# Kernel tuning notes

Hardware: AMD Instinct MI355X
Metric: run time of the kernel (lower is better)

Reference implementation:

```python
import jax, jax.numpy as jnp
import numpy as np

N_HEAD, D_K = 8, 16

def _ln(x, g, b):
    m = jnp.mean(x, -1, keepdims=True)
    v = jnp.var(x, -1, keepdims=True)
    return (x - m) * jax.lax.rsqrt(v + 1e-5) * g + b

def _enc_layer(x, wq, bq, wk, bk, wv, bv, wo, bo, g1, be1, cw1, cb1, cw2, cb2, g2, be2):
    B, L, D = x.shape
    q = (x @ wq + bq).reshape(B, L, N_HEAD, D_K)
    k = (x @ wk + bk).reshape(B, L, N_HEAD, D_K)
    v = (x @ wv + bv).reshape(B, L, N_HEAD, D_K)
    attn = jnp.einsum('blhd,bmhd->bhlm', q, k) / jnp.sqrt(jnp.float32(D_K))
    attn = jax.nn.softmax(attn, axis=-1)
    o = jnp.einsum('bhlm,bmhd->blhd', attn, v).reshape(B, L, -1)
    x = _ln(o @ wo + bo + x, g1, be1)          # post-LN residual (MHA)
    h = jax.nn.relu(x @ cw1 + cb1)             # 1x1 conv == linear
    return _ln(h @ cw2 + cb2 + x, g2, be2)     # post-LN residual (FFN)

def setup_inputs() -> dict:
    key = jax.random.key(0)
    ks = jax.random.split(key, 20)
    N, D, NNZ = 100000, 128, 2000000
    B, L, NL, DI = 32, 256, 2, 512
    s = 0.02
    inp = {}
    inp['ego'] = jax.random.normal(ks[0], (N, D), jnp.float32)
    inp['vals'] = jax.random.uniform(ks[1], (NNZ,), jnp.float32) / 20.0  # ~normalized adj values
    inp['W1'] = jax.random.normal(ks[2], (D, D), jnp.float32) * s
    inp['b1'] = jnp.zeros((D,), jnp.float32)
    inp['W2'] = jax.random.normal(ks[3], (D, D), jnp.float32) * s
    inp['b2'] = jnp.zeros((D,), jnp.float32)
    inp['enc_in'] = jax.random.normal(ks[4], (B, L, D), jnp.float32)
    inp['wq'] = jax.random.normal(ks[5], (NL, D, D), jnp.float32) * s
    inp['bq'] = jnp.zeros((NL, D), jnp.float32)
    inp['wk'] = jax.random.normal(ks[6], (NL, D, D), jnp.float32) * s
    inp['bk'] = jnp.zeros((NL, D), jnp.float32)
    inp['wv'] = jax.random.normal(ks[7], (NL, D, D), jnp.float32) * s
    inp['bv'] = jnp.zeros((NL, D), jnp.float32)
    inp['wo'] = jax.random.normal(ks[8], (NL, D, D), jnp.float32) * s
    inp['bo'] = jnp.zeros((NL, D), jnp.float32)
    inp['ln1_g'] = jnp.ones((NL, D), jnp.float32)
    inp['ln1_b'] = jnp.zeros((NL, D), jnp.float32)
    inp['cw1'] = jax.random.normal(ks[9], (NL, D, DI), jnp.float32) * s
    inp['cb1'] = jnp.zeros((NL, DI), jnp.float32)
    inp['cw2'] = jax.random.normal(ks[10], (NL, DI, D), jnp.float32) * s
    inp['cb2'] = jnp.zeros((NL, D), jnp.float32)
    inp['ln2_g'] = jnp.ones((NL, D), jnp.float32)
    inp['ln2_b'] = jnp.zeros((NL, D), jnp.float32)
    inp['rows'] = jnp.sort(jax.random.randint(ks[11], (NNZ,), 0, N, jnp.int32))
    inp['cols'] = jax.random.randint(ks[12], (NNZ,), 0, N, jnp.int32)
    return inp

def reference(ego, vals, W1, b1, W2, b2, enc_in, wq, bq, wk, bk, wv, bv, wo, bo,
              ln1_g, ln1_b, cw1, cb1, cw2, cb2, ln2_g, ln2_b, rows, cols):
    N = ego.shape[0]
    # sparse A_in @ ego  (COO SpMM via gather + segment_sum)
    side = jax.ops.segment_sum(vals[:, None] * ego[cols], rows, num_segments=N)
    # bi-interaction aggregator (dropout=identity in eval)
    sum_emb = jax.nn.leaky_relu((ego + side) @ W1 + b1)
    bi_emb = jax.nn.leaky_relu((ego * side) @ W2 + b2)
    agg = sum_emb + bi_emb
    # transformer encoder over edge sequences
    x = enc_in
    for i in range(wq.shape[0]):
        x = _enc_layer(x, wq[i], bq[i], wk[i], bk[i], wv[i], bv[i], wo[i], bo[i],
                       ln1_g[i], ln1_b[i], cw1[i], cb1[i], cw2[i], cb2[i], ln2_g[i], ln2_b[i])
    return (agg, x)
```

## Files before the change

kernel.cpp:

```cpp
#include <hip/hip_runtime.h>

typedef __attribute__((ext_vector_type(8))) short bf16x8;
typedef __attribute__((ext_vector_type(4))) float f32x4;

__device__ __forceinline__ unsigned short f2b(float f) {
    union { float f; unsigned int i; } u; u.f = f;
    return (unsigned short)((u.i + 0x7FFFu + ((u.i >> 16) & 1u)) >> 16);
}
__device__ __forceinline__ unsigned int packbf2(float a, float b) {
    return (unsigned int)f2b(a) | ((unsigned int)f2b(b) << 16);
}

__device__ __forceinline__ void spmm_block(
    const unsigned int* __restrict__ egob, const float* __restrict__ vals,
    const int* __restrict__ rows, const int* __restrict__ cols,
    float* __restrict__ side, int nnz, int blk)
{
    int tid = threadIdx.x;
    int wave = tid >> 6, lane = tid & 63;
    int e0 = blk * 256 + wave * 64;
    if (e0 >= nnz) return;

    int idx = e0 + lane;
    int last = nnz - 1;
    bool ok = idx < nnz;
    int safe = ok ? idx : last;
    int my_row = rows[safe];
    int my_col = cols[safe];
    float my_val = ok ? vals[safe] : 0.f;

    unsigned int pre[16];
    #pragma unroll
    for (int j = 0; j < 16; ++j) {
        unsigned int c = (unsigned int)__builtin_amdgcn_readlane(my_col, j);
        pre[j] = *(egob + ((size_t)c << 6) + lane);
    }

    float ax = 0.f, ay = 0.f;
    int cur = __builtin_amdgcn_readlane(my_row, 0);
    #pragma unroll
    for (int e = 0; e < 64; ++e) {
        int r = __builtin_amdgcn_readlane(my_row, e);
        float vv = __int_as_float(__builtin_amdgcn_readlane(__float_as_int(my_val), e));
        unsigned int u = pre[e & 15];
        if (e < 48) {
            unsigned int c = (unsigned int)__builtin_amdgcn_readlane(my_col, e + 16);
            pre[e & 15] = *(egob + ((size_t)c << 6) + lane);
        }
        if (r != cur) {
            atomicAdd(&side[(size_t)cur * 128 + lane * 2], ax);
            atomicAdd(&side[(size_t)cur * 128 + lane * 2 + 1], ay);
            ax = 0.f; ay = 0.f; cur = r;
        }
        ax = fmaf(vv, __uint_as_float(u << 16), ax);
        ay = fmaf(vv, __uint_as_float(u & 0xFFFF0000u), ay);
    }
    atomicAdd(&side[(size_t)cur * 128 + lane * 2], ax);
    atomicAdd(&side[(size_t)cur * 128 + lane * 2 + 1], ay);
}

#define LDAB 40

__device__ __forceinline__ void gemm2_core(
    const float* __restrict__ A, const float* __restrict__ W,
    const float* __restrict__ bias, const float* __restrict__ R,
    const float* __restrict__ g, const float* __restrict__ bta,
    float* __restrict__ C, int M, int N, int K, int act,
    int bm, int bn, unsigned short* As, unsigned short* Bs,
    float* redS, float* redSS)
{
    int tid = threadIdx.x, wave = tid >> 6, lane = tid & 63;
    int lm = lane & 15, quad = lane >> 4;
    int wm = wave >> 1, wn = wave & 1;

    f32x4 acc[2][4];
    #pragma unroll
    for (int i = 0; i < 2; ++i)
        #pragma unroll
        for (int j = 0; j < 4; ++j) acc[i][j] = (f32x4)(0.f);

    for (int k0 = 0; k0 < K; k0 += 32) {
        {
            int m = tid >> 2, kc = (tid & 3) * 8;
            const float* p = A + (size_t)(bm + m) * K + k0 + kc;
            float4 a0 = *(const float4*)p, a1 = *(const float4*)(p + 4);
            uint4 pk;
            pk.x = packbf2(a0.x, a0.y); pk.y = packbf2(a0.z, a0.w);
            pk.z = packbf2(a1.x, a1.y); pk.w = packbf2(a1.z, a1.w);
            *(uint4*)&As[m * LDAB + kc] = pk;
        }
        {
            int nn = tid & 127, kh = (tid >> 7) * 16;
            const float* p = W + (size_t)(k0 + kh) * N + bn + nn;
            float w[16];
            #pragma unroll
            for (int j = 0; j < 16; ++j) w[j] = p[(size_t)j * N];
            uint4 pk;
            pk.x = packbf2(w[0], w[1]);  pk.y = packbf2(w[2], w[3]);
            pk.z = packbf2(w[4], w[5]);  pk.w = packbf2(w[6], w[7]);
            *(uint4*)&Bs[nn * LDAB + kh] = pk;
            pk.x = packbf2(w[8], w[9]);  pk.y = packbf2(w[10], w[11]);
            pk.z = packbf2(w[12], w[13]); pk.w = packbf2(w[14], w[15]);
            *(uint4*)&Bs[nn * LDAB + kh + 8] = pk;
        }
        __syncthreads();
        bf16x8 af[2], bfr[4];
        #pragma unroll
        for (int mi = 0; mi < 2; ++mi)
            af[mi] = *(bf16x8*)&As[(wm * 32 + mi * 16 + lm) * LDAB + quad * 8];
        #pragma unroll
        for (int ni = 0; ni < 4; ++ni)
            bfr[ni] = *(bf16x8*)&Bs[(wn * 64 + ni * 16 + lm) * LDAB + quad * 8];
        #pragma unroll
        for (int mi = 0; mi < 2; ++mi)
            #pragma unroll
            for (int ni = 0; ni < 4; ++ni)
                acc[mi][ni] = __builtin_amdgcn_mfma_f32_16x16x32_bf16(
                    af[mi], bfr[ni], acc[mi][ni], 0, 0, 0);
        __syncthreads();
    }

    #pragma unroll
    for (int mi = 0; mi < 2; ++mi) {
        #pragma unroll
        for (int r = 0; r < 4; ++r) {
            int row = bm + wm * 32 + mi * 16 + quad * 4 + r;
            #pragma unroll
            for (int ni = 0; ni < 4; ++ni) {
                int col = bn + wn * 64 + ni * 16 + lm;
                float v = acc[mi][ni][r] + bias[col];
                if (R) v += R[(size_t)row * N + col];
                if (act) v = fmaxf(v, 0.f);
                acc[mi][ni][r] = v;
            }
        }
    }

    if (g) {
        #pragma unroll
        for (int mi = 0; mi < 2; ++mi) {
            #pragma unroll
            for (int r = 0; r < 4; ++r) {
                float s = 0.f, ss = 0.f;
                #pragma unroll
                for (int ni = 0; ni < 4; ++ni) {
                    float v = acc[mi][ni][r];
                    s += v; ss = fmaf(v, v, ss);
                }
                #pragma unroll
                for (int off = 1; off < 16; off <<= 1) {
                    s  += __shfl_xor(s, off, 64);
                    ss += __shfl_xor(ss, off, 64);
                }
                if (lm == 0) {
                    int lr = wm * 32 + mi * 16 + quad * 4 + r;
                    redS[wn * 64 + lr] = s;
                    redSS[wn * 64 + lr] = ss;
                }
            }
        }
        __syncthreads();
        #pragma unroll
        for (int mi = 0; mi < 2; ++mi) {
            #pragma unroll
            for (int r = 0; r < 4; ++r) {
                int lr = wm * 32 + mi * 16 + quad * 4 + r;
                int row = bm + lr;
                float s = redS[lr] + redS[64 + lr];
                float ss = redSS[lr] + redSS[64 + lr];
                float mean = s * (1.f / 128.f);
                float var = ss * (1.f / 128.f) - mean * mean;
                float rstd = rsqrtf(var + 1e-5f);
                #pragma unroll
                for (int ni = 0; ni < 4; ++ni) {
                    int col = wn * 64 + ni * 16 + lm;
                    float y = (acc[mi][ni][r] - mean) * rstd * g[col] + bta[col];
                    C[(size_t)row * 128 + col] = y;
                }
            }
        }
    } else {
        #pragma unroll
        for (int mi = 0; mi < 2; ++mi) {
            #pragma unroll
            for (int r = 0; r < 4; ++r) {
                int row = bm + wm * 32 + mi * 16 + quad * 4 + r;
                #pragma unroll
                for (int ni = 0; ni < 4; ++ni) {
                    int col = bn + wn * 64 + ni * 16 + lm;
                    C[(size_t)row * N + col] = acc[mi][ni][r];
                }
            }
        }
    }
}

__device__ __forceinline__ void bi_core2(
    const float* __restrict__ ego, const float* __restrict__ side,
    const float* __restrict__ W1, const float* __restrict__ b1,
    const float* __restrict__ W2, const float* __restrict__ b2,
    float* __restrict__ out, int M, int bm,
    unsigned short* Us, unsigned short* Ms,
    unsigned short* W1s, unsigned short* W2s)
{
    int tid = threadIdx.x, wave = tid >> 6, lane = tid & 63;
    int lm = lane & 15, quad = lane >> 4;
    int wm = wave >> 1, wn = wave & 1;

    f32x4 acc1[2][4], acc2[2][4];
    #pragma unroll
    for (int i = 0; i < 2; ++i)
        #pragma unroll
        for (int j = 0; j < 4; ++j) { acc1[i][j] = (f32x4)(0.f); acc2[i][j] = (f32x4)(0.f); }

    for (int k0 = 0; k0 < 128; k0 += 32) {
        {
            int m = tid >> 2, kc = (tid & 3) * 8;
            int gm = bm + m;
            float e[8], s[8];
            if (gm < M) {
                const float* pe = ego + (size_t)gm * 128 + k0 + kc;
                const float* ps = side + (size_t)gm * 128 + k0 + kc;
                float4 e0 = *(const float4*)pe, e1 = *(const float4*)(pe + 4);
                float4 s0 = *(const float4*)ps, s1 = *(const float4*)(ps + 4);
                e[0]=e0.x; e[1]=e0.y; e[2]=e0.z; e[3]=e0.w;
                e[4]=e1.x; e[5]=e1.y; e[6]=e1.z; e[7]=e1.w;
                s[0]=s0.x; s[1]=s0.y; s[2]=s0.z; s[3]=s0.w;
                s[4]=s1.x; s[5]=s1.y; s[6]=s1.z; s[7]=s1.w;
            } else {
                #pragma unroll
                for (int j = 0; j < 8; ++j) { e[j] = 0.f; s[j] = 0.f; }
            }
            uint4 pu, pm;
            pu.x = packbf2(e[0]+s[0], e[1]+s[1]); pu.y = packbf2(e[2]+s[2], e[3]+s[3]);
            pu.z = packbf2(e[4]+s[4], e[5]+s[5]); pu.w = packbf2(e[6]+s[6], e[7]+s[7]);
            pm.x = packbf2(e[0]*s[0], e[1]*s[1]); pm.y = packbf2(e[2]*s[2], e[3]*s[3]);
            pm.z = packbf2(e[4]*s[4], e[5]*s[5]); pm.w = packbf2(e[6]*s[6], e[7]*s[7]);
            *(uint4*)&Us[m * LDAB + kc] = pu;
            *(uint4*)&Ms[m * LDAB + kc] = pm;
        }
        {
            int nn = tid & 127, kh = (tid >> 7) * 16;
            const float* p1 = W1 + (size_t)(k0 + kh) * 128 + nn;
            const float* p2 = W2 + (size_t)(k0 + kh) * 128 + nn;
            float wa[16], wb[16];
            #pragma unroll
            for (int j = 0; j < 16; ++j) { wa[j] = p1[(size_t)j * 128]; wb[j] = p2[(size_t)j * 128]; }
            uint4 pk;
            pk.x = packbf2(wa[0], wa[1]);  pk.y = packbf2(wa[2], wa[3]);
            pk.z = packbf2(wa[4], wa[5]);  pk.w = packbf2(wa[6], wa[7]);
            *(uint4*)&W1s[nn * LDAB + kh] = pk;
            pk.x = packbf2(wa[8], wa[9]);  pk.y = packbf2(wa[10], wa[11]);
            pk.z = packbf2(wa[12], wa[13]); pk.w = packbf2(wa[14], wa[15]);
            *(uint4*)&W1s[nn * LDAB + kh + 8] = pk;
            pk.x = packbf2(wb[0], wb[1]);  pk.y = packbf2(wb[2], wb[3]);
            pk.z = packbf2(wb[4], wb[5]);  pk.w = packbf2(wb[6], wb[7]);
            *(uint4*)&W2s[nn * LDAB + kh] = pk;
            pk.x = packbf2(wb[8], wb[9]);  pk.y = packbf2(wb[10], wb[11]);
            pk.z = packbf2(wb[12], wb[13]); pk.w = packbf2(wb[14], wb[15]);
            *(uint4*)&W2s[nn * LDAB + kh + 8] = pk;
        }
        __syncthreads();
        bf16x8 au[2], am[2], bf1[4], bf2[4];
        #pragma unroll
        for (int mi = 0; mi < 2; ++mi) {
            au[mi] = *(bf16x8*)&Us[(wm * 32 + mi * 16 + lm) * LDAB + quad * 8];
            am[mi] = *(bf16x8*)&Ms[(wm * 32 + mi * 16 + lm) * LDAB + quad * 8];
        }
        #pragma unroll
        for (int ni = 0; ni < 4; ++ni) {
            bf1[ni] = *(bf16x8*)&W1s[(wn * 64 + ni * 16 + lm) * LDAB + quad * 8];
            bf2[ni] = *(bf16x8*)&W2s[(wn * 64 + ni * 16 + lm) * LDAB + quad * 8];
        }
        #pragma unroll
        for (int mi = 0; mi < 2; ++mi)
            #pragma unroll
            for (int ni = 0; ni < 4; ++ni) {
                acc1[mi][ni] = __builtin_amdgcn_mfma_f32_16x16x32_bf16(
                    au[mi], bf1[ni], acc1[mi][ni], 0, 0, 0);
                acc2[mi][ni] = __builtin_amdgcn_mfma_f32_16x16x32_bf16(
                    am[mi], bf2[ni], acc2[mi][ni], 0, 0, 0);
            }
        __syncthreads();
    }
    #pragma unroll
    for (int mi = 0; mi < 2; ++mi) {
        #pragma unroll
        for (int r = 0; r < 4; ++r) {
            int row = bm + wm * 32 + mi * 16 + quad * 4 + r;
            if (row < M) {
                #pragma unroll
                for (int ni = 0; ni < 4; ++ni) {
                    int col = wn * 64 + ni * 16 + lm;
                    float v1 = acc1[mi][ni][r] + b1[col];
                    v1 = v1 > 0.f ? v1 : 0.01f * v1;
                    float v2 = acc2[mi][ni][r] + b2[col];
                    v2 = v2 > 0.f ? v2 : 0.01f * v2;
                    out[(size_t)row * 128 + col] = v1 + v2;
                }
            }
        }
    }
}


__global__ __launch_bounds__(256) void qkv2_pre(
    const float* __restrict__ A,
    const float* __restrict__ wq, const float* __restrict__ wk, const float* __restrict__ wv,
    const float* __restrict__ bq, const float* __restrict__ bk, const float* __restrict__ bv,
    float* __restrict__ Q, float* __restrict__ Ko, float* __restrict__ V, int M, int encGy,
    float* __restrict__ side, int Nn,
    const float* __restrict__ ego, unsigned int* __restrict__ egob,
    int encN, int ZB, int CB)
{
    __shared__ unsigned short As[64 * LDAB];
    __shared__ unsigned short Bs[128 * LDAB];
    __shared__ float redS[128], redSS[128];
    int gid = blockIdx.x;
    int tid = threadIdx.x;
    if (gid >= encN) {
        int j = gid - encN;
        if (j < ZB) {
            size_t n4 = (size_t)Nn * 32;
            float4 z = make_float4(0.f, 0.f, 0.f, 0.f);
            for (size_t i = (size_t)j * 256 + tid; i < n4; i += (size_t)ZB * 256)
                ((float4*)side)[i] = z;
        } else {
            int c = j - ZB;
            size_t n4 = (size_t)Nn * 32;
            for (size_t i = (size_t)c * 256 + tid; i < n4; i += (size_t)CB * 256) {
                float4 a = *(const float4*)(ego + i * 4);
                uint2 p;
                p.x = packbf2(a.x, a.y);
                p.y = packbf2(a.z, a.w);
                *(uint2*)(egob + i * 2) = p;
            }
        }
        return;
    }
    int sel = gid / encGy, by = gid % encGy;
    const float* W = (sel == 0) ? wq : (sel == 1) ? wk : wv;
    const float* b = (sel == 0) ? bq : (sel == 1) ? bk : bv;
    float* C = (sel == 0) ? Q : (sel == 1) ? Ko : V;
    gemm2_core(A, W, b, nullptr, nullptr, nullptr, C, M, 128, 128, 0,
               by * 64, 0, As, Bs, redS, redSS);
}

__global__ __launch_bounds__(256) void qkv2_spmm(
    const float* __restrict__ A,
    const float* __restrict__ wq, const float* __restrict__ wk, const float* __restrict__ wv,
    const float* __restrict__ bq, const float* __restrict__ bk, const float* __restrict__ bv,
    float* __restrict__ Q, float* __restrict__ Ko, float* __restrict__ V, int M, int encGy,
    const unsigned int* __restrict__ egob, const float* __restrict__ vals,
    const int* __restrict__ rows, const int* __restrict__ cols,
    float* __restrict__ side, int nnz, int spmmBase, int encN)
{
    __shared__ unsigned short As[64 * LDAB];
    __shared__ unsigned short Bs[128 * LDAB];
    __shared__ float redS[128], redSS[128];
    int gid = blockIdx.x;
    if (gid >= encN) {
        spmm_block(egob, vals, rows, cols, side, nnz, spmmBase + gid - encN);
        return;
    }
    int sel = gid / encGy, by = gid % encGy;
    const float* W = (sel == 0) ? wq : (sel == 1) ? wk : wv;
    const float* b = (sel == 0) ? bq : (sel == 1) ? bk : bv;
    float* C = (sel == 0) ? Q : (sel == 1) ? Ko : V;
    gemm2_core(A, W, b, nullptr, nullptr, nullptr, C, M, 128, 128, 0,
               by * 64, 0, As, Bs, redS, redSS);
}

__global__ __launch_bounds__(256) void gemm2_spmm(
    const float* __restrict__ A, const float* __restrict__ W,
    const float* __restrict__ bias, const float* __restrict__ R,
    const float* __restrict__ g, const float* __restrict__ bta,
    float* __restrict__ C, int M, int N, int K, int act, int encGy,
    const unsigned int* __restrict__ egob, const float* __restrict__ vals,
    const int* __restrict__ rows, const int* __restrict__ cols,
    float* __restrict__ side, int nnz, int spmmBase, int encN)
{
    __shared__ unsigned short As[64 * LDAB];
    __shared__ unsigned short Bs[128 * LDAB];
    __shared__ float redS[128], redSS[128];
    int gid = blockIdx.x;
    if (gid >= encN) {
        spmm_block(egob, vals, rows, cols, side, nnz, spmmBase + gid - encN);
        return;
    }
    int bx = gid / encGy, by = gid % encGy;
    gemm2_core(A, W, bias, R, g, bta, C, M, N, K, act,
               by * 64, bx * 128, As, Bs, redS, redSS);
}

__global__ __launch_bounds__(256) void gemm2_bi2(
    const float* __restrict__ A, const float* __restrict__ W,
    const float* __restrict__ bias, const float* __restrict__ R,
    const float* __restrict__ g, const float* __restrict__ bta,
    float* __restrict__ C, int M, int N, int K, int act, int encGy, int encN,
    const float* __restrict__ ego, const float* __restrict__ side,
    const float* __restrict__ W1, const float* __restrict__ b1,
    const float* __restrict__ W2, const float* __restrict__ b2,
    float* __restrict__ out, int Mbi, int biBase)
{
    __shared__ char smem[30720];
    int gid = blockIdx.x;
    if (gid < encN) {
        unsigned short* As = (unsigned short*)smem;
        unsigned short* Bs = (unsigned short*)(smem + 5120);
        float* redS  = (float*)(smem + 15360);
        float* redSS = (float*)(smem + 15360 + 512);
        int bx = gid / encGy, by = gid % encGy;
        gemm2_core(A, W, bias, R, g, bta, C, M, N, K, act,
                   by * 64, bx * 128, As, Bs, redS, redSS);
    } else {
        int bb = biBase + (gid - encN);
        unsigned short* Us  = (unsigned short*)smem;
        unsigned short* Ms  = (unsigned short*)(smem + 5120);
        unsigned short* W1s = (unsigned short*)(smem + 10240);
        unsigned short* W2s = (unsigned short*)(smem + 20480);
        bi_core2(ego, side, W1, b1, W2, b2, out, Mbi, bb * 64, Us, Ms, W1s, W2s);
    }
}

__device__ __forceinline__ void attn_block(
    const float* __restrict__ q, const float* __restrict__ k,
    const float* __restrict__ v, float* __restrict__ o, int NH,
    int bh, float* Ks, float* Vs)
{
    const int L = 256, DK = 16;
    int b = bh / NH, h = bh % NH;
    int tid = threadIdx.x;

    size_t qbase = ((size_t)(b * L + tid) * NH + h) * DK;
    float qr[16];
    #pragma unroll
    for (int d4 = 0; d4 < 4; ++d4) {
        float4 t = *(const float4*)(q + qbase + d4 * 4);
        qr[d4*4+0] = t.x * 0.25f; qr[d4*4+1] = t.y * 0.25f;
        qr[d4*4+2] = t.z * 0.25f; qr[d4*4+3] = t.w * 0.25f;
    }
    float acc[16];
    #pragma unroll
    for (int d = 0; d < 16; ++d) acc[d] = 0.f;
    float mmax = -1e30f, ssum = 0.f;

    for (int c0 = 0; c0 < L; c0 += 128) {
        __syncthreads();
        for (int i = tid; i < 128 * 4; i += 256) {
            int ll = i >> 2, d4 = (i & 3) * 4;
            size_t gg = ((size_t)(b * L + c0 + ll) * NH + h) * DK + d4;
            *(float4*)&Ks[ll * 16 + d4] = *(const float4*)(k + gg);
            *(float4*)&Vs[ll * 16 + d4] = *(const float4*)(v + gg);
        }
        __syncthreads();

        for (int kk = 0; kk < 128; ++kk) {
            float dot = 0.f;
            #pragma unroll
            for (int d4 = 0; d4 < 4; ++d4) {
                float4 kv = *(const float4*)&Ks[kk * 16 + d4 * 4];
                dot = fmaf(qr[d4*4+0], kv.x, dot);
                dot = fmaf(qr[d4*4+1], kv.y, dot);
                dot = fmaf(qr[d4*4+2], kv.z, dot);
                dot = fmaf(qr[d4*4+3], kv.w, dot);
            }
            if (dot > mmax) {
                float alpha = __expf(mmax - dot);
                ssum *= alpha;
                #pragma unroll
                for (int d = 0; d < 16; ++d) acc[d] *= alpha;
                mmax = dot;
            }
            float p = __expf(dot - mmax);
            ssum += p;
            #pragma unroll
            for (int d4 = 0; d4 < 4; ++d4) {
                float4 vv = *(const float4*)&Vs[kk * 16 + d4 * 4];
                acc[d4*4+0] = fmaf(p, vv.x, acc[d4*4+0]);
                acc[d4*4+1] = fmaf(p, vv.y, acc[d4*4+1]);
                acc[d4*4+2] = fmaf(p, vv.z, acc[d4*4+2]);
                acc[d4*4+3] = fmaf(p, vv.w, acc[d4*4+3]);
            }
        }
    }
    float inv = 1.f / ssum;
    #pragma unroll
    for (int d4 = 0; d4 < 4; ++d4) {
        float4 t;
        t.x = acc[d4*4+0] * inv; t.y = acc[d4*4+1] * inv;
        t.z = acc[d4*4+2] * inv; t.w = acc[d4*4+3] * inv;
        *(float4*)(o + qbase + d4 * 4) = t;
    }
}

__global__ __launch_bounds__(256) void attn_spmm(
    const float* __restrict__ q, const float* __restrict__ k,
    const float* __restrict__ v, float* __restrict__ o, int NH,
    const unsigned int* __restrict__ egob, const float* __restrict__ vals,
    const int* __restrict__ rows, const int* __restrict__ cols,
    float* __restrict__ side, int nnz, int spmmBase, int encN)
{
    __shared__ float Ks[128 * 16];
    __shared__ float Vs[128 * 16];
    int gid = blockIdx.x;
    if (gid >= encN) {
        spmm_block(egob, vals, rows, cols, side, nnz, spmmBase + gid - encN);
        return;
    }
    attn_block(q, k, v, o, NH, gid, Ks, Vs);
}

extern "C" void kernel_launch(void* const* d_in, const int* in_sizes, int n_in,
                              void* d_out, int out_size, void* d_ws, size_t ws_size,
                              hipStream_t stream) {
    const float* ego    = (const float*)d_in[0];
    const float* vals   = (const float*)d_in[1];
    const float* W1     = (const float*)d_in[2];
    const float* b1     = (const float*)d_in[3];
    const float* W2     = (const float*)d_in[4];
    const float* b2     = (const float*)d_in[5];
    const float* enc_in = (const float*)d_in[6];
    const float* wq  = (const float*)d_in[7];
    const float* bq  = (const float*)d_in[8];
    const float* wk  = (const float*)d_in[9];
    const float* bk  = (const float*)d_in[10];
    const float* wv  = (const float*)d_in[11];
    const float* bv  = (const float*)d_in[12];
    const float* wo  = (const float*)d_in[13];
    const float* bo  = (const float*)d_in[14];
    const float* ln1_g = (const float*)d_in[15];
    const float* ln1_b = (const float*)d_in[16];
    const float* cw1 = (const float*)d_in[17];
    const float* cb1 = (const float*)d_in[18];
    const float* cw2 = (const float*)d_in[19];
    const float* cb2 = (const float*)d_in[20];
    const float* ln2_g = (const float*)d_in[21];
    const float* ln2_b = (const float*)d_in[22];
    const int* rows = (const int*)d_in[23];
    const int* cols = (const int*)d_in[24];

    const int D = 128, DI = 512, NH = 8, L = 256;
    const int Nn   = in_sizes[0] / D;
    const int nnz  = in_sizes[1];
    const int NL   = in_sizes[7] / (D * D);
    const int Menc = in_sizes[6] / D;
    const int Bb   = Menc / L;

    float* ws = (float*)d_ws;
    size_t off = 0;
    float* side = ws + off; off += (size_t)Nn * D;
    float* Qb = ws + off; off += (size_t)Menc * D;
    float* Kb = ws + off; off += (size_t)Menc * D;
    float* Vb = ws + off; off += (size_t)Menc * D;
    float* Ob = ws + off; off += (size_t)Menc * D;
    float* XA = ws + off; off += (size_t)Menc * D;
    float* XB = ws + off; off += (size_t)Menc * D;
    float* Hb = ws + off; off += (size_t)Menc * DI;
    unsigned int* egob = (unsigned int*)(ws + off); off += (size_t)Nn * (D / 2);

    float* outAgg = (float*)d_out;
    float* outX   = (float*)d_out + (size_t)Nn * D;

    const int spmmBlocks = (nnz + 255) / 256;
    const int nSpmmStages = 5 * NL - 3;
    const int perS = (spmmBlocks + nSpmmStages - 1) / nSpmmStages;
    const int biTiles = (Nn + 63) / 64;
    const int perB = (biTiles + 1) / 2;
    const int biStart = 5 * NL - 1;
    const int encGy = Menc / 64;
    const int ZB = 512, CB = 1024;
    int sidx = 0, sci = 0, bci = 0;

    const float* x = enc_in;
    for (int i = 0; i < NL; ++i) {
        const size_t wOff = (size_t)i * D * D;
        int base, cnt;
        #define SPMM_CHUNK base = sci * perS; cnt = spmmBlocks - base; \
                           if (cnt < 0) cnt = 0; if (cnt > perS) cnt = perS; sci++
        #define BI_CHUNK   base = bci * perB; cnt = biTiles - base; \
                           if (cnt < 0) cnt = 0; if (cnt > perB) cnt = perB; bci++

        sidx++;
        if (sidx == 1) {
            qkv2_pre<<<3 * encGy + ZB + CB, 256, 0, stream>>>(
                x, wq + wOff, wk + wOff, wv + wOff,
                bq + (size_t)i * D, bk + (size_t)i * D, bv + (size_t)i * D,
                Qb, Kb, Vb, Menc, encGy,
                side, Nn, ego, egob, 3 * encGy, ZB, CB);
        } else {
            SPMM_CHUNK;
            qkv2_spmm<<<3 * encGy + cnt, 256, 0, stream>>>(
                x, wq + wOff, wk + wOff, wv + wOff,
                bq + (size_t)i * D, bk + (size_t)i * D, bv + (size_t)i * D,
                Qb, Kb, Vb, Menc, encGy,
                egob, vals, rows, cols, side, nnz, base, 3 * encGy);
        }

        sidx++;
        SPMM_CHUNK;
        attn_spmm<<<Bb * NH + cnt, 256, 0, stream>>>(
            Qb, Kb, Vb, Ob, NH,
            egob, vals, rows, cols, side, nnz, base, Bb * NH);

        sidx++;
        SPMM_CHUNK;
        gemm2_spmm<<<encGy + cnt, 256, 0, stream>>>(
            Ob, wo + wOff, bo + (size_t)i * D, x,
            ln1_g + (size_t)i * D, ln1_b + (size_t)i * D, XA, Menc, D, D, 0, encGy,
            egob, vals, rows, cols, side, nnz, base, encGy);

        sidx++;
        if (sidx >= biStart) {
            BI_CHUNK;
            gemm2_bi2<<<4 * encGy + cnt, 256, 0, stream>>>(
                XA, cw1 + (size_t)i * D * DI, cb1 + (size_t)i * DI, nullptr,
                nullptr, nullptr, Hb, Menc, DI, D, 1, encGy, 4 * encGy,
                ego, side, W1, b1, W2, b2, outAgg, Nn, base);
        } else {
            SPMM_CHUNK;
            gemm2_spmm<<<4 * encGy + cnt, 256, 0, stream>>>(
                XA, cw1 + (size_t)i * D * DI, cb1 + (size_t)i * DI, nullptr,
                nullptr, nullptr, Hb, Menc, DI, D, 1, encGy,
                egob, vals, rows, cols, side, nnz, base, 4 * encGy);
        }

        sidx++;
        float* dst = (i == NL - 1) ? outX : XB;
        if (sidx >= biStart) {
            BI_CHUNK;
            gemm2_bi2<<<encGy + cnt, 256, 0, stream>>>(
                Hb, cw2 + (size_t)i * DI * D, cb2 + (size_t)i * D, XA,
                ln2_g + (size_t)i * D, ln2_b + (size_t)i * D, dst, Menc, D, DI, 0,
                encGy, encGy,
                ego, side, W1, b1, W2, b2, outAgg, Nn, base);
        } else {
            SPMM_CHUNK;
            gemm2_spmm<<<encGy + cnt, 256, 0, stream>>>(
                Hb, cw2 + (size_t)i * DI * D, cb2 + (size_t)i * D, XA,
                ln2_g + (size_t)i * D, ln2_b + (size_t)i * D, dst, Menc, D, DI, 0, encGy,
                egob, vals, rows, cols, side, nnz, base, encGy);
        }
        #undef SPMM_CHUNK
        #undef BI_CHUNK
        x = XB;
    }
}
```

Before: 475.6 us.

## Pre-transpose bi-interaction weights to bf16 once and read fragments from global

Adds a prologue stage inside the first fused kernel that converts W1 and W2 into transposed bf16 copies in workspace. The bi-interaction tiles then load their MFMA B fragments straight from these global copies instead of reloading, converting and staging the fp32 weights through shared memory in every tile. The K loop goes from 4 steps of 32 to 2 steps of 64, which halves the barriers, and shared memory per block drops from 30 KB to 18 KB. In exchange, B fragments are now read from global/L2 on every k-step, and the first kernel takes on some extra work.

```diff
diff --git a/kernel.cpp b/kernel.cpp
--- a/kernel.cpp
+++ b/kernel.cpp
@@ -60,6 +60,7 @@
 }
 
 #define LDAB 40
+#define LDBI 72
 
 __device__ __forceinline__ void gemm2_core(
     const float* __restrict__ A, const float* __restrict__ W,
@@ -195,13 +196,12 @@
     }
 }
 
-__device__ __forceinline__ void bi_core2(
+__device__ __forceinline__ void bi_core3(
     const float* __restrict__ ego, const float* __restrict__ side,
-    const float* __restrict__ W1, const float* __restrict__ b1,
-    const float* __restrict__ W2, const float* __restrict__ b2,
+    const unsigned short* __restrict__ W1t, const unsigned short* __restrict__ W2t,
+    const float* __restrict__ b1, const float* __restrict__ b2,
     float* __restrict__ out, int M, int bm,
-    unsigned short* Us, unsigned short* Ms,
-    unsigned short* W1s, unsigned short* W2s)
+    unsigned short* Us, unsigned short* Ms)
 {
     int tid = threadIdx.x, wave = tid >> 6, lane = tid & 63;
     int lm = lane & 15, quad = lane >> 4;
@@ -213,75 +213,71 @@
         #pragma unroll
         for (int j = 0; j < 4; ++j) { acc1[i][j] = (f32x4)(0.f); acc2[i][j] = (f32x4)(0.f); }
 
-    for (int k0 = 0; k0 < 128; k0 += 32) {
+    #pragma unroll
+    for (int h = 0; h < 2; ++h) {
+        int k0 = h * 64;
+        if (h) __syncthreads();
         {
-            int m = tid >> 2, kc = (tid & 3) * 8;
+            int m = tid >> 2, kc = (tid & 3) * 16;
             int gm = bm + m;
-            float e[8], s[8];
+            float e[16], s[16];
             if (gm < M) {
                 const float* pe = ego + (size_t)gm * 128 + k0 + kc;
                 const float* ps = side + (size_t)gm * 128 + k0 + kc;
-                float4 e0 = *(const float4*)pe, e1 = *(const float4*)(pe + 4);
-                float4 s0 = *(const float4*)ps, s1 = *(const float4*)(ps + 4);
-                e[0]=e0.x; e[1]=e0.y; e[2]=e0.z; e[3]=e0.w;
-                e[4]=e1.x; e[5]=e1.y; e[6]=e1.z; e[7]=e1.w;
-                s[0]=s0.x; s[1]=s0.y; s[2]=s0.z; s[3]=s0.w;
-                s[4]=s1.x; s[5]=s1.y; s[6]=s1.z; s[7]=s1.w;
+                #pragma unroll
+                for (int j = 0; j < 4; ++j) {
+                    float4 ev = *(const float4*)(pe + j * 4);
+                    float4 sv = *(const float4*)(ps + j * 4);
+                    e[j*4+0] = ev.x; e[j*4+1] = ev.y; e[j*4+2] = ev.z; e[j*4+3] = ev.w;
+                    s[j*4+0] = sv.x; s[j*4+1] = sv.y; s[j*4+2] = sv.z; s[j*4+3] = sv.w;
+                }
             } else {
                 #pragma unroll
-                for (int j = 0; j < 8; ++j) { e[j] = 0.f; s[j] = 0.f; }
-            }
-            uint4 pu, pm;
-            pu.x = packbf2(e[0]+s[0], e[1]+s[1]); pu.y = packbf2(e[2]+s[2], e[3]+s[3]);
-            pu.z = packbf2(e[4]+s[4], e[5]+s[5]); pu.w = packbf2(e[6]+s[6], e[7]+s[7]);
-            pm.x = packbf2(e[0]*s[0], e[1]*s[1]); pm.y = packbf2(e[2]*s[2], e[3]*s[3]);
-            pm.z = packbf2(e[4]*s[4], e[5]*s[5]); pm.w = packbf2(e[6]*s[6], e[7]*s[7]);
-            *(uint4*)&Us[m * LDAB + kc] = pu;
-            *(uint4*)&Ms[m * LDAB + kc] = pm;
-        }
-        {
-            int nn = tid & 127, kh = (tid >> 7) * 16;
-            const float* p1 = W1 + (size_t)(k0 + kh) * 128 + nn;
-            const float* p2 = W2 + (size_t)(k0 + kh) * 128 + nn;
-            float wa[16], wb[16];
-            #pragma unroll
-            for (int j = 0; j < 16; ++j) { wa[j] = p1[(size_t)j * 128]; wb[j] = p2[(size_t)j * 128]; }
-            uint4 pk;
-            pk.x = packbf2(wa[0], wa[1]);  pk.y = packbf2(wa[2], wa[3]);
-            pk.z = packbf2(wa[4], wa[5]);  pk.w = packbf2(wa[6], wa[7]);
-            *(uint4*)&W1s[nn * LDAB + kh] = pk;
-            pk.x = packbf2(wa[8], wa[9]);  pk.y = packbf2(wa[10], wa[11]);
-            pk.z = packbf2(wa[12], wa[13]); pk.w = packbf2(wa[14], wa[15]);
-            *(uint4*)&W1s[nn * LDAB + kh + 8] = pk;
-            pk.x = packbf2(wb[0], wb[1]);  pk.y = packbf2(wb[2], wb[3]);
-            pk.z = packbf2(wb[4], wb[5]);  pk.w = packbf2(wb[6], wb[7]);
-            *(uint4*)&W2s[nn * LDAB + kh] = pk;
-            pk.x = packbf2(wb[8], wb[9]);  pk.y = packbf2(wb[10], wb[11]);
-            pk.z = packbf2(wb[12], wb[13]); pk.w = packbf2(wb[14], wb[15]);
-            *(uint4*)&W2s[nn * LDAB + kh + 8] = pk;
+                for (int j = 0; j < 16; ++j) { e[j] = 0.f; s[j] = 0.f; }
+            }
+            #pragma unroll
+            for (int j = 0; j < 2; ++j) {
+                int b0 = j * 8;
+                uint4 pu, pv;
+                pu.x = packbf2(e[b0+0]+s[b0+0], e[b0+1]+s[b0+1]);
+                pu.y = packbf2(e[b0+2]+s[b0+2], e[b0+3]+s[b0+3]);
+                pu.z = packbf2(e[b0+4]+s[b0+4], e[b0+5]+s[b0+5]);
+                pu.w = packbf2(e[b0+6]+s[b0+6], e[b0+7]+s[b0+7]);
+                pv.x = packbf2(e[b0+0]*s[b0+0], e[b0+1]*s[b0+1]);
+                pv.y = packbf2(e[b0+2]*s[b0+2], e[b0+3]*s[b0+3]);
+                pv.z = packbf2(e[b0+4]*s[b0+4], e[b0+5]*s[b0+5]);
+                pv.w = packbf2(e[b0+6]*s[b0+6], e[b0+7]*s[b0+7]);
+                *(uint4*)&Us[m * LDBI + kc + b0] = pu;
+                *(uint4*)&Ms[m * LDBI + kc + b0] = pv;
+            }
         }
         __syncthreads();
-        bf16x8 au[2], am[2], bf1[4], bf2[4];
-        #pragma unroll
-        for (int mi = 0; mi < 2; ++mi) {
-            au[mi] = *(bf16x8*)&Us[(wm * 32 + mi * 16 + lm) * LDAB + quad * 8];
-            am[mi] = *(bf16x8*)&Ms[(wm * 32 + mi * 16 + lm) * LDAB + quad * 8];
-        }
-        #pragma unroll
-        for (int ni = 0; ni < 4; ++ni) {
-            bf1[ni] = *(bf16x8*)&W1s[(wn * 64 + ni * 16 + lm) * LDAB + quad * 8];
-            bf2[ni] = *(bf16x8*)&W2s[(wn * 64 + ni * 16 + lm) * LDAB + quad * 8];
-        }
-        #pragma unroll
-        for (int mi = 0; mi < 2; ++mi)
+        #pragma unroll
+        for (int ks = 0; ks < 2; ++ks) {
+            bf16x8 au[2], am[2], bf1[4], bf2[4];
+            #pragma unroll
+            for (int mi = 0; mi < 2; ++mi) {
+                int off = (wm * 32 + mi * 16 + lm) * LDBI + ks * 32 + quad * 8;
+                au[mi] = *(bf16x8*)&Us[off];
+                am[mi] = *(bf16x8*)&Ms[off];
+            }
             #pragma unroll
             for (int ni = 0; ni < 4; ++ni) {
-                acc1[mi][ni] = __builtin_amdgcn_mfma_f32_16x16x32_bf16(
-                    au[mi], bf1[ni], acc1[mi][ni], 0, 0, 0);
-                acc2[mi][ni] = __builtin_amdgcn_mfma_f32_16x16x32_bf16(
-                    am[mi], bf2[ni], acc2[mi][ni], 0, 0, 0);
-            }
-        __syncthreads();
+                size_t n = (size_t)(wn * 64 + ni * 16 + lm);
+                size_t koff = n * 128 + k0 + ks * 32 + quad * 8;
+                bf1[ni] = *(const bf16x8*)(W1t + koff);
+                bf2[ni] = *(const bf16x8*)(W2t + koff);
+            }
+            #pragma unroll
+            for (int mi = 0; mi < 2; ++mi)
+                #pragma unroll
+                for (int ni = 0; ni < 4; ++ni) {
+                    acc1[mi][ni] = __builtin_amdgcn_mfma_f32_16x16x32_bf16(
+                        au[mi], bf1[ni], acc1[mi][ni], 0, 0, 0);
+                    acc2[mi][ni] = __builtin_amdgcn_mfma_f32_16x16x32_bf16(
+                        am[mi], bf2[ni], acc2[mi][ni], 0, 0, 0);
+                }
+        }
     }
     #pragma unroll
     for (int mi = 0; mi < 2; ++mi) {
@@ -311,7 +307,9 @@
     float* __restrict__ Q, float* __restrict__ Ko, float* __restrict__ V, int M, int encGy,
     float* __restrict__ side, int Nn,
     const float* __restrict__ ego, unsigned int* __restrict__ egob,
-    int encN, int ZB, int CB)
+    const float* __restrict__ W1, const float* __restrict__ W2,
+    unsigned short* __restrict__ W1t, unsigned short* __restrict__ W2t,
+    int encN, int ZB, int CB, int WTB)
 {
     __shared__ unsigned short As[64 * LDAB];
     __shared__ unsigned short Bs[128 * LDAB];
@@ -325,7 +323,7 @@
             float4 z = make_float4(0.f, 0.f, 0.f, 0.f);
             for (size_t i = (size_t)j * 256 + tid; i < n4; i += (size_t)ZB * 256)
                 ((float4*)side)[i] = z;
-        } else {
+        } else if (j < ZB + CB) {
             int c = j - ZB;
             size_t n4 = (size_t)Nn * 32;
             for (size_t i = (size_t)c * 256 + tid; i < n4; i += (size_t)CB * 256) {
@@ -335,6 +333,22 @@
                 p.y = packbf2(a.z, a.w);
                 *(uint2*)(egob + i * 2) = p;
             }
+        } else {
+            int c = j - ZB - CB;
+            for (int ch = c * 256 + tid; ch < 4096; ch += WTB * 256) {
+                int w = ch >> 11, rem = ch & 2047;
+                int n = rem >> 4, k8 = rem & 15;
+                const float* src = w ? W2 : W1;
+                unsigned short* dst = w ? W2t : W1t;
+                float t[8];
+                #pragma unroll
+                for (int jj = 0; jj < 8; ++jj)
+                    t[jj] = src[(size_t)(k8 * 8 + jj) * 128 + n];
+                uint4 pk;
+                pk.x = packbf2(t[0], t[1]); pk.y = packbf2(t[2], t[3]);
+                pk.z = packbf2(t[4], t[5]); pk.w = packbf2(t[6], t[7]);
+                *(uint4*)&dst[(size_t)n * 128 + k8 * 8] = pk;
+            }
         }
         return;
     }
@@ -393,17 +407,17 @@
                by * 64, bx * 128, As, Bs, redS, redSS);
 }
 
-__global__ __launch_bounds__(256) void gemm2_bi2(
+__global__ __launch_bounds__(256) void gemm2_bi3(
     const float* __restrict__ A, const float* __restrict__ W,
     const float* __restrict__ bias, const float* __restrict__ R,
     const float* __restrict__ g, const float* __restrict__ bta,
     float* __restrict__ C, int M, int N, int K, int act, int encGy, int encN,
     const float* __restrict__ ego, const float* __restrict__ side,
-    const float* __restrict__ W1, const float* __restrict__ b1,
-    const float* __restrict__ W2, const float* __restrict__ b2,
+    const unsigned short* __restrict__ W1t, const unsigned short* __restrict__ W2t,
+    const float* __restrict__ b1, const float* __restrict__ b2,
     float* __restrict__ out, int Mbi, int biBase)
 {
-    __shared__ char smem[30720];
+    __shared__ char smem[18432];
     int gid = blockIdx.x;
     if (gid < encN) {
         unsigned short* As = (unsigned short*)smem;
@@ -415,11 +429,9 @@
                    by * 64, bx * 128, As, Bs, redS, redSS);
     } else {
         int bb = biBase + (gid - encN);
-        unsigned short* Us  = (unsigned short*)smem;
-        unsigned short* Ms  = (unsigned short*)(smem + 5120);
-        unsigned short* W1s = (unsigned short*)(smem + 10240);
-        unsigned short* W2s = (unsigned short*)(smem + 20480);
-        bi_core2(ego, side, W1, b1, W2, b2, out, Mbi, bb * 64, Us, Ms, W1s, W2s);
+        unsigned short* Us = (unsigned short*)smem;
+        unsigned short* Ms = (unsigned short*)(smem + 9216);
+        bi_core3(ego, side, W1t, W2t, b1, b2, out, Mbi, bb * 64, Us, Ms);
     }
 }
 
@@ -558,6 +570,8 @@
     float* XB = ws + off; off += (size_t)Menc * D;
     float* Hb = ws + off; off += (size_t)Menc * DI;
     unsigned int* egob = (unsigned int*)(ws + off); off += (size_t)Nn * (D / 2);
+    unsigned short* W1t = (unsigned short*)(ws + off); off += (size_t)D * D / 2;
+    unsigned short* W2t = (unsigned short*)(ws + off); off += (size_t)D * D / 2;
 
     float* outAgg = (float*)d_out;
     float* outX   = (float*)d_out + (size_t)Nn * D;
@@ -569,7 +583,7 @@
     const int perB = (biTiles + 1) / 2;
     const int biStart = 5 * NL - 1;
     const int encGy = Menc / 64;
-    const int ZB = 512, CB = 1024;
+    const int ZB = 512, CB = 1024, WTB = 16;
     int sidx = 0, sci = 0, bci = 0;
 
     const float* x = enc_in;
@@ -583,11 +597,11 @@
 
         sidx++;
         if (sidx == 1) {
-            qkv2_pre<<<3 * encGy + ZB + CB, 256, 0, stream>>>(
+            qkv2_pre<<<3 * encGy + ZB + CB + WTB, 256, 0, stream>>>(
                 x, wq + wOff, wk + wOff, wv + wOff,
                 bq + (size_t)i * D, bk + (size_t)i * D, bv + (size_t)i * D,
                 Qb, Kb, Vb, Menc, encGy,
-                side, Nn, ego, egob, 3 * encGy, ZB, CB);
+                side, Nn, ego, egob, W1, W2, W1t, W2t, 3 * encGy, ZB, CB, WTB);
         } else {
             SPMM_CHUNK;
             qkv2_spmm<<<3 * encGy + cnt, 256, 0, stream>>>(
@@ -613,10 +627,10 @@
         sidx++;
         if (sidx >= biStart) {
             BI_CHUNK;
-            gemm2_bi2<<<4 * encGy + cnt, 256, 0, stream>>>(
+            gemm2_bi3<<<4 * encGy + cnt, 256, 0, stream>>>(
                 XA, cw1 + (size_t)i * D * DI, cb1 + (size_t)i * DI, nullptr,
                 nullptr, nullptr, Hb, Menc, DI, D, 1, encGy, 4 * encGy,
-                ego, side, W1, b1, W2, b2, outAgg, Nn, base);
+                ego, side, W1t, W2t, b1, b2, outAgg, Nn, base);
         } else {
             SPMM_CHUNK;
             gemm2_spmm<<<4 * encGy + cnt, 256, 0, stream>>>(
@@ -629,11 +643,11 @@
         float* dst = (i == NL - 1) ? outX : XB;
         if (sidx >= biStart) {
             BI_CHUNK;
-            gemm2_bi2<<<encGy + cnt, 256, 0, stream>>>(
+            gemm2_bi3<<<encGy + cnt, 256, 0, stream>>>(
                 Hb, cw2 + (size_t)i * DI * D, cb2 + (size_t)i * D, XA,
                 ln2_g + (size_t)i * D, ln2_b + (size_t)i * D, dst, Menc, D, DI, 0,
                 encGy, encGy,
-                ego, side, W1, b1, W2, b2, outAgg, Nn, base);
+                ego, side, W1t, W2t, b1, b2, outAgg, Nn, base);
         } else {
             SPMM_CHUNK;
             gemm2_spmm<<<encGy + cnt, 256, 0, stream>>>(
```

After: 481.9 us. No clear change (+1.3%).
